# Kernel tuning notes

Measured on AMD Instinct MI355X. Metric: run time of the kernel, lower is better.

The kernel has to match this reference:

```python
import jax, jax.numpy as jnp
import numpy as np

B, H = 8192, 768


def _mk_linear(key, fan_in, fan_out):
    k1, k2 = jax.random.split(key)
    lim = 1.0 / np.sqrt(fan_in)
    W = jax.random.uniform(k1, (fan_out, fan_in), jnp.float32, -lim, lim)
    b = jax.random.uniform(k2, (fan_out,), jnp.float32, -lim, lim)
    return W, b


def setup_inputs() -> dict:
    key = jax.random.key(0)
    ks = jax.random.split(key, 6)
    modal_a = jax.random.normal(ks[0], (B, H), jnp.float32)
    modal_b = jax.random.normal(ks[1], (B, H), jnp.float32)
    W1m, b1m = _mk_linear(ks[2], H, H)
    W2m, b2m = _mk_linear(ks[3], H, H)
    W1v, b1v = _mk_linear(ks[4], H, H)
    W2v, b2v = _mk_linear(ks[5], H, H)
    return {"modal_a": modal_a, "modal_b": modal_b,
            "W1m": W1m, "b1m": b1m, "W2m": W2m, "b2m": b2m,
            "W1v": W1v, "b1v": b1v, "W2v": W2v, "b2v": b2v}


def reference(modal_a, modal_b, W1m, b1m, W2m, b2m, W1v, b1v, W2v, b2v):
    # mlp_mu: Linear -> Tanh -> Linear
    mu = jnp.tanh(modal_a @ W1m.T + b1m) @ W2m.T + b2m              # [B,H]
    # mlp_logvar: Linear -> Tanh -> Linear -> Tanh
    logvar = jnp.tanh(jnp.tanh(modal_a @ W1v.T + b1v) @ W2v.T + b2v)  # [B,H]
    inv_var = jnp.exp(-logvar)

    positive = -(mu - modal_b) ** 2 * 0.5 * inv_var                  # [B,H]

    # mean_j (mu[j] - mu[i])^2 = E[mu^2] - 2*mu[i]*E[mu] + mu[i]^2  (per feature dim)
    # Algebraic reduction of the O(B^2*H) tile in the original code.
    mu_mean = jnp.mean(mu, axis=0)                                   # [H]
    mu_sq_mean = jnp.mean(mu * mu, axis=0)                           # [H]
    pair_sq = mu_sq_mean - 2.0 * mu * mu_mean + mu * mu              # [B,H]
    negative = -pair_sq * 0.5 * inv_var                              # [B,H]

    pos_sum = jnp.sum(positive, axis=-1)                             # [B]
    neg_sum = jnp.sum(negative, axis=-1)                             # [B]
    lld = jnp.mean(pos_sum)
    bound = jnp.mean(pos_sum - neg_sum)
    return (lld, bound)
```

## Files before the change

### kernel.cpp

```cpp
#include <hip/hip_runtime.h>
#include <hip/hip_fp8.h>
#include <math.h>

typedef float v4f __attribute__((ext_vector_type(4)));

static constexpr int Bn = 8192;
static constexpr int Hn = 768;
static constexpr float invB = 1.0f / 8192.0f;

__device__ __forceinline__ unsigned char cvt_e4m3(float x) {
    __hip_fp8_e4m3 t(x);
    return t.__x;
}

__device__ __forceinline__ unsigned pack4_e4m3(float4 f) {
    return (unsigned)cvt_e4m3(f.x)
         | ((unsigned)cvt_e4m3(f.y) << 8)
         | ((unsigned)cvt_e4m3(f.z) << 16)
         | ((unsigned)cvt_e4m3(f.w) << 24);
}

__device__ __forceinline__ float fast_tanh(float x) {
    float xc = fminf(fmaxf(x, -15.0f), 15.0f);
    float e = __expf(2.0f * xc);
    float r = __builtin_amdgcn_rcpf(e + 1.0f);
    return 1.0f - 2.0f * r;
}

__global__ void prep_w(const float* __restrict__ W1m, const float* __restrict__ W2m,
                       const float* __restrict__ W1v, const float* __restrict__ W2v,
                       unsigned char* __restrict__ W1m_f8, unsigned char* __restrict__ W2m_f8,
                       unsigned char* __restrict__ W1v_f8, unsigned char* __restrict__ W2v_f8,
                       float* __restrict__ zbuf, int nzero) {
    const int tid = blockIdx.x * blockDim.x + threadIdx.x;
    if (tid < nzero) zbuf[tid] = 0.0f;
    constexpr int W4 = Hn * Hn / 4;
    const int total = 4 * W4;
    const int stride = gridDim.x * blockDim.x;
    for (int i = tid; i < total; i += stride) {
        int w = i / W4, j = i - w * W4;
        const float* s = (w == 0) ? W1m : (w == 1) ? W2m : (w == 2) ? W1v : W2v;
        unsigned char* d = (w == 0) ? W1m_f8 : (w == 1) ? W2m_f8 : (w == 2) ? W1v_f8 : W2v_f8;
        float4 v = ((const float4*)s)[j];
        ((unsigned*)d)[j] = pack4_e4m3(v);
    }
}

__launch_bounds__(1024, 4)
__global__ void club_fused(const float* __restrict__ A_g,
                           const unsigned char* __restrict__ W1m, const unsigned char* __restrict__ W1v,
                           const unsigned char* __restrict__ W2m, const unsigned char* __restrict__ W2v,
                           const float* __restrict__ b1m, const float* __restrict__ b1v,
                           const float* __restrict__ b2m, const float* __restrict__ b2v,
                           const float* __restrict__ mb,
                           float* __restrict__ cs, float* __restrict__ cs2,
                           float* __restrict__ siv, float* __restrict__ sivmu,
                           float* __restrict__ accum, float* __restrict__ outp) {
    __shared__ __align__(16) unsigned char Hm[32 * 768];
    __shared__ __align__(16) unsigned char Xs[32 * 768];
    const int t = threadIdx.x;
    const int strip0 = blockIdx.x * 32;

    for (int c = t; c < 1536; c += 1024) {
        const int row = c / 48, cc = c - row * 48;
        const float* src = A_g + (size_t)(strip0 + row) * Hn + cc * 16;
        float4 f0 = *(const float4*)(src + 0);
        float4 f1 = *(const float4*)(src + 4);
        float4 f2 = *(const float4*)(src + 8);
        float4 f3 = *(const float4*)(src + 12);
        uint4 p;
        p.x = pack4_e4m3(f0); p.y = pack4_e4m3(f1);
        p.z = pack4_e4m3(f2); p.w = pack4_e4m3(f3);
        *(uint4*)&Xs[row * 768 + ((cc ^ (row & 15)) << 4)] = p;
    }
    __syncthreads();

    const int w = t >> 6, lane = t & 63;
    const int lr = lane & 15, quad = lane >> 4;
    const int wc0 = w * 48;

    v4f am[3][2] = {}, av[3][2] = {};
    {
        const unsigned char* __restrict__ pWm = W1m + (size_t)(wc0 + lr) * Hn + quad * 16;
        const unsigned char* __restrict__ pWv = W1v + (size_t)(wc0 + lr) * Hn + quad * 16;
#pragma unroll
        for (int ms = 0; ms < 12; ++ms) {
            ulonglong2 wmf[3], wvf[3], af[2];
#pragma unroll
            for (int ct = 0; ct < 3; ++ct) {
                wmf[ct] = *(const ulonglong2*)(pWm + ct * (16 * Hn) + ms * 64);
                wvf[ct] = *(const ulonglong2*)(pWv + ct * (16 * Hn) + ms * 64);
            }
#pragma unroll
            for (int rt = 0; rt < 2; ++rt) {
                const int row_ = rt * 16 + lr;
                const int k_ = ms * 4 + quad;
                af[rt] = *(const ulonglong2*)&Xs[row_ * 768 + ((k_ ^ (row_ & 15)) << 4)];
            }
#pragma unroll
            for (int ct = 0; ct < 3; ++ct)
#pragma unroll
                for (int rt = 0; rt < 2; ++rt) {
                    am[ct][rt] = __builtin_amdgcn_mfma_f32_16x16x32_fp8_fp8((long)wmf[ct].x, (long)af[rt].x, am[ct][rt], 0, 0, 0);
                    av[ct][rt] = __builtin_amdgcn_mfma_f32_16x16x32_fp8_fp8((long)wvf[ct].x, (long)af[rt].x, av[ct][rt], 0, 0, 0);
                }
#pragma unroll
            for (int ct = 0; ct < 3; ++ct)
#pragma unroll
                for (int rt = 0; rt < 2; ++rt) {
                    am[ct][rt] = __builtin_amdgcn_mfma_f32_16x16x32_fp8_fp8((long)wmf[ct].y, (long)af[rt].y, am[ct][rt], 0, 0, 0);
                    av[ct][rt] = __builtin_amdgcn_mfma_f32_16x16x32_fp8_fp8((long)wvf[ct].y, (long)af[rt].y, av[ct][rt], 0, 0, 0);
                }
        }
    }

    __syncthreads();

#pragma unroll
    for (int ct = 0; ct < 3; ++ct) {
        const float4 bbm = *(const float4*)&b1m[wc0 + ct * 16 + quad * 4];
        const float4 bbv = *(const float4*)&b1v[wc0 + ct * 16 + quad * 4];
        const int cc = w * 3 + ct;
#pragma unroll
        for (int rt = 0; rt < 2; ++rt) {
            const int row = rt * 16 + lr;
            v4f a = am[ct][rt];
            unsigned pm = (unsigned)cvt_e4m3(fast_tanh(a[0] + bbm.x))
                        | ((unsigned)cvt_e4m3(fast_tanh(a[1] + bbm.y)) << 8)
                        | ((unsigned)cvt_e4m3(fast_tanh(a[2] + bbm.z)) << 16)
                        | ((unsigned)cvt_e4m3(fast_tanh(a[3] + bbm.w)) << 24);
            v4f b = av[ct][rt];
            unsigned pv = (unsigned)cvt_e4m3(fast_tanh(b[0] + bbv.x))
                        | ((unsigned)cvt_e4m3(fast_tanh(b[1] + bbv.y)) << 8)
                        | ((unsigned)cvt_e4m3(fast_tanh(b[2] + bbv.z)) << 16)
                        | ((unsigned)cvt_e4m3(fast_tanh(b[3] + bbv.w)) << 24);
            const int off = row * 768 + ((cc ^ (row & 15)) << 4) + quad * 4;
            *(unsigned*)&Hm[off] = pm;
            *(unsigned*)&Xs[off] = pv;
        }
    }
    __syncthreads();

    v4f cm[2][3] = {}, cv[2][3] = {};
    {
        const unsigned char* __restrict__ pWm = W2m + (size_t)(wc0 + lr) * Hn + quad * 16;
        const unsigned char* __restrict__ pWv = W2v + (size_t)(wc0 + lr) * Hn + quad * 16;
#pragma unroll
        for (int ms = 0; ms < 12; ++ms) {
            ulonglong2 wmf[3], wvf[3], amf[2], avf[2];
#pragma unroll
            for (int ct = 0; ct < 3; ++ct) {
                wmf[ct] = *(const ulonglong2*)(pWm + ct * (16 * Hn) + ms * 64);
                wvf[ct] = *(const ulonglong2*)(pWv + ct * (16 * Hn) + ms * 64);
            }
#pragma unroll
            for (int rt = 0; rt < 2; ++rt) {
                const int row_ = rt * 16 + lr;
                const int k_ = ms * 4 + quad;
                const int off_ = row_ * 768 + ((k_ ^ (row_ & 15)) << 4);
                amf[rt] = *(const ulonglong2*)&Hm[off_];
                avf[rt] = *(const ulonglong2*)&Xs[off_];
            }
#pragma unroll
            for (int rt = 0; rt < 2; ++rt)
#pragma unroll
                for (int ct = 0; ct < 3; ++ct) {
                    cm[rt][ct] = __builtin_amdgcn_mfma_f32_16x16x32_fp8_fp8((long)amf[rt].x, (long)wmf[ct].x, cm[rt][ct], 0, 0, 0);
                    cv[rt][ct] = __builtin_amdgcn_mfma_f32_16x16x32_fp8_fp8((long)avf[rt].x, (long)wvf[ct].x, cv[rt][ct], 0, 0, 0);
                }
#pragma unroll
            for (int rt = 0; rt < 2; ++rt)
#pragma unroll
                for (int ct = 0; ct < 3; ++ct) {
                    cm[rt][ct] = __builtin_amdgcn_mfma_f32_16x16x32_fp8_fp8((long)amf[rt].y, (long)wmf[ct].y, cm[rt][ct], 0, 0, 0);
                    cv[rt][ct] = __builtin_amdgcn_mfma_f32_16x16x32_fp8_fp8((long)avf[rt].y, (long)wvf[ct].y, cv[rt][ct], 0, 0, 0);
                }
        }
    }

    float pos = 0.f, q = 0.f;
#pragma unroll
    for (int ct = 0; ct < 3; ++ct) {
        const int col = wc0 + ct * 16 + lr;
        const float bmc = b2m[col], bvc = b2v[col];
        float c1 = 0.f, c2 = 0.f, c3 = 0.f, c4 = 0.f;
#pragma unroll
        for (int rt = 0; rt < 2; ++rt) {
#pragma unroll
            for (int r = 0; r < 4; ++r) {
                const int row = strip0 + rt * 16 + quad * 4 + r;
                float mu = cm[rt][ct][r] + bmc;
                float tv = fast_tanh(cv[rt][ct][r] + bvc);
                float iv = __expf(-tv);
                float mbv = mb[(size_t)row * Hn + col];
                float d = mu - mbv;
                pos += iv * d * d;
                q   += iv * mu * mu;
                c1 += mu; c2 += mu * mu; c3 += iv; c4 += iv * mu;
            }
        }
        c1 += __shfl_xor(c1, 16); c1 += __shfl_xor(c1, 32);
        c2 += __shfl_xor(c2, 16); c2 += __shfl_xor(c2, 32);
        c3 += __shfl_xor(c3, 16); c3 += __shfl_xor(c3, 32);
        c4 += __shfl_xor(c4, 16); c4 += __shfl_xor(c4, 32);
        if (quad == 0) {
            atomicAdd(&cs[col], c1);
            atomicAdd(&cs2[col], c2);
            atomicAdd(&siv[col], c3);
            atomicAdd(&sivmu[col], c4);
        }
    }
    for (int off = 32; off > 0; off >>= 1) {
        pos += __shfl_down(pos, off);
        q   += __shfl_down(q, off);
    }
    __shared__ float redP[16], redQ[16];
    if (lane == 0) { redP[w] = pos; redQ[w] = q; }
    __syncthreads();
    __shared__ int is_last;
    if (t == 0) {
        float sp = 0.f, sq = 0.f;
#pragma unroll
        for (int i = 0; i < 16; ++i) { sp += redP[i]; sq += redQ[i]; }
        atomicAdd(&accum[0], sp);
        atomicAdd(&accum[1], sq);
        __threadfence();
        unsigned old = atomicAdd((unsigned int*)&accum[3], 1u);
        is_last = (old == gridDim.x - 1) ? 1 : 0;
    }
    __syncthreads();
    if (is_last) {
        float term = 0.f;
        for (int h = t; h < Hn; h += 1024) {
            float v1 = atomicAdd(&cs[h], 0.0f);
            float v2 = atomicAdd(&cs2[h], 0.0f);
            float v3 = atomicAdd(&siv[h], 0.0f);
            float v4 = atomicAdd(&sivmu[h], 0.0f);
            term += v3 * v2 - 2.0f * v4 * v1;
        }
        for (int off = 32; off > 0; off >>= 1) term += __shfl_down(term, off);
        __shared__ float redT[16];
        if (lane == 0) redT[w] = term;
        __syncthreads();
        if (t == 0) {
            float T = 0.f;
#pragma unroll
            for (int i = 0; i < 16; ++i) T += redT[i];
            float P = atomicAdd(&accum[0], 0.0f);
            float Q = atomicAdd(&accum[1], 0.0f);
            float pos_sum = -0.5f * P;
            float neg_sum = -0.5f * (T * invB + Q);
            outp[0] = pos_sum * invB;
            outp[1] = (pos_sum - neg_sum) * invB;
        }
    }
}

extern "C" void kernel_launch(void* const* d_in, const int* in_sizes, int n_in,
                              void* d_out, int out_size, void* d_ws, size_t ws_size,
                              hipStream_t stream) {
    const float* modal_a = (const float*)d_in[0];
    const float* modal_b = (const float*)d_in[1];
    const float* W1m = (const float*)d_in[2];
    const float* b1m = (const float*)d_in[3];
    const float* W2m = (const float*)d_in[4];
    const float* b2m = (const float*)d_in[5];
    const float* W1v = (const float*)d_in[6];
    const float* b1v = (const float*)d_in[7];
    const float* W2v = (const float*)d_in[8];
    const float* b2v = (const float*)d_in[9];
    float* out = (float*)d_out;

    char* ws = (char*)d_ws;
    constexpr size_t szW8 = (size_t)Hn * Hn;
    unsigned char* W1m_f8 = (unsigned char*)(ws);
    unsigned char* W2m_f8 = (unsigned char*)(ws + szW8);
    unsigned char* W1v_f8 = (unsigned char*)(ws + 2 * szW8);
    unsigned char* W2v_f8 = (unsigned char*)(ws + 3 * szW8);
    float* cs     = (float*)(ws + 4 * szW8);
    float* cs2    = cs + Hn;
    float* siv    = cs + 2 * Hn;
    float* sivmu  = cs + 3 * Hn;
    float* accum  = cs + 4 * Hn;

    prep_w<<<576, 256, 0, stream>>>(W1m, W2m, W1v, W2v,
                                    W1m_f8, W2m_f8, W1v_f8, W2v_f8,
                                    cs, 4 * Hn + 8);

    club_fused<<<dim3(Bn / 32), 1024, 0, stream>>>(
        modal_a, W1m_f8, W1v_f8, W2m_f8, W2v_f8,
        b1m, b1v, b2m, b2v, modal_b,
        cs, cs2, siv, sivmu, accum, out);
}
```

Before: 188.0 us.

## Merge weight-quantization prep into main kernel with cooperative grid sync

```diff
diff --git a/kernel.cpp b/kernel.cpp
--- a/kernel.cpp
+++ b/kernel.cpp
@@ -1,4 +1,5 @@
 #include <hip/hip_runtime.h>
+#include <hip/hip_cooperative_groups.h>
 #include <hip/hip_fp8.h>
 #include <math.h>
 
@@ -27,39 +28,36 @@
     return 1.0f - 2.0f * r;
 }
 
-__global__ void prep_w(const float* __restrict__ W1m, const float* __restrict__ W2m,
-                       const float* __restrict__ W1v, const float* __restrict__ W2v,
-                       unsigned char* __restrict__ W1m_f8, unsigned char* __restrict__ W2m_f8,
-                       unsigned char* __restrict__ W1v_f8, unsigned char* __restrict__ W2v_f8,
-                       float* __restrict__ zbuf, int nzero) {
-    const int tid = blockIdx.x * blockDim.x + threadIdx.x;
-    if (tid < nzero) zbuf[tid] = 0.0f;
-    constexpr int W4 = Hn * Hn / 4;
-    const int total = 4 * W4;
-    const int stride = gridDim.x * blockDim.x;
-    for (int i = tid; i < total; i += stride) {
-        int w = i / W4, j = i - w * W4;
-        const float* s = (w == 0) ? W1m : (w == 1) ? W2m : (w == 2) ? W1v : W2v;
-        unsigned char* d = (w == 0) ? W1m_f8 : (w == 1) ? W2m_f8 : (w == 2) ? W1v_f8 : W2v_f8;
-        float4 v = ((const float4*)s)[j];
-        ((unsigned*)d)[j] = pack4_e4m3(v);
-    }
-}
-
 __launch_bounds__(1024, 4)
-__global__ void club_fused(const float* __restrict__ A_g,
-                           const unsigned char* __restrict__ W1m, const unsigned char* __restrict__ W1v,
-                           const unsigned char* __restrict__ W2m, const unsigned char* __restrict__ W2v,
-                           const float* __restrict__ b1m, const float* __restrict__ b1v,
-                           const float* __restrict__ b2m, const float* __restrict__ b2v,
-                           const float* __restrict__ mb,
-                           float* __restrict__ cs, float* __restrict__ cs2,
-                           float* __restrict__ siv, float* __restrict__ sivmu,
-                           float* __restrict__ accum, float* __restrict__ outp) {
+__global__ void club_all(const float* __restrict__ A_g, const float* __restrict__ mb,
+                         const float* __restrict__ W1m_f, const float* __restrict__ W2m_f,
+                         const float* __restrict__ W1v_f, const float* __restrict__ W2v_f,
+                         const float* __restrict__ b1m, const float* __restrict__ b1v,
+                         const float* __restrict__ b2m, const float* __restrict__ b2v,
+                         unsigned char* __restrict__ W1m8, unsigned char* __restrict__ W2m8,
+                         unsigned char* __restrict__ W1v8, unsigned char* __restrict__ W2v8,
+                         float* __restrict__ cs, float* __restrict__ cs2,
+                         float* __restrict__ siv, float* __restrict__ sivmu,
+                         float* __restrict__ accum, float* __restrict__ outp) {
     __shared__ __align__(16) unsigned char Hm[32 * 768];
     __shared__ __align__(16) unsigned char Xs[32 * 768];
     const int t = threadIdx.x;
     const int strip0 = blockIdx.x * 32;
+
+    {
+        const int gtid = blockIdx.x * 1024 + t;
+        if (gtid < 4 * Hn + 8) cs[gtid] = 0.0f;
+        constexpr int W4 = Hn * Hn / 4;
+        for (int i = gtid; i < 4 * W4; i += 256 * 1024) {
+            int w = i / W4, j = i - w * W4;
+            const float* s = (w == 0) ? W1m_f : (w == 1) ? W2m_f : (w == 2) ? W1v_f : W2v_f;
+            unsigned char* d = (w == 0) ? W1m8 : (w == 1) ? W2m8 : (w == 2) ? W1v8 : W2v8;
+            float4 v = ((const float4*)s)[j];
+            ((unsigned*)d)[j] = pack4_e4m3(v);
+        }
+    }
+    __threadfence();
+    cooperative_groups::this_grid().sync();
 
     for (int c = t; c < 1536; c += 1024) {
         const int row = c / 48, cc = c - row * 48;
@@ -81,8 +79,8 @@
 
     v4f am[3][2] = {}, av[3][2] = {};
     {
-        const unsigned char* __restrict__ pWm = W1m + (size_t)(wc0 + lr) * Hn + quad * 16;
-        const unsigned char* __restrict__ pWv = W1v + (size_t)(wc0 + lr) * Hn + quad * 16;
+        const unsigned char* __restrict__ pWm = W1m8 + (size_t)(wc0 + lr) * Hn + quad * 16;
+        const unsigned char* __restrict__ pWv = W1v8 + (size_t)(wc0 + lr) * Hn + quad * 16;
 #pragma unroll
         for (int ms = 0; ms < 12; ++ms) {
             ulonglong2 wmf[3], wvf[3], af[2];
@@ -143,8 +141,8 @@
 
     v4f cm[2][3] = {}, cv[2][3] = {};
     {
-        const unsigned char* __restrict__ pWm = W2m + (size_t)(wc0 + lr) * Hn + quad * 16;
-        const unsigned char* __restrict__ pWv = W2v + (size_t)(wc0 + lr) * Hn + quad * 16;
+        const unsigned char* __restrict__ pWm = W2m8 + (size_t)(wc0 + lr) * Hn + quad * 16;
+        const unsigned char* __restrict__ pWv = W2v8 + (size_t)(wc0 + lr) * Hn + quad * 16;
 #pragma unroll
         for (int ms = 0; ms < 12; ++ms) {
             ulonglong2 wmf[3], wvf[3], amf[2], avf[2];
@@ -283,12 +281,13 @@
     float* sivmu  = cs + 3 * Hn;
     float* accum  = cs + 4 * Hn;
 
-    prep_w<<<576, 256, 0, stream>>>(W1m, W2m, W1v, W2v,
-                                    W1m_f8, W2m_f8, W1v_f8, W2v_f8,
-                                    cs, 4 * Hn + 8);
-
-    club_fused<<<dim3(Bn / 32), 1024, 0, stream>>>(
-        modal_a, W1m_f8, W1v_f8, W2m_f8, W2v_f8,
-        b1m, b1v, b2m, b2v, modal_b,
-        cs, cs2, siv, sivmu, accum, out);
-}
+    void* args[] = { (void*)&modal_a, (void*)&modal_b,
+                     (void*)&W1m, (void*)&W2m, (void*)&W1v, (void*)&W2v,
+                     (void*)&b1m, (void*)&b1v, (void*)&b2m, (void*)&b2v,
+                     (void*)&W1m_f8, (void*)&W2m_f8, (void*)&W1v_f8, (void*)&W2v_f8,
+                     (void*)&cs, (void*)&cs2, (void*)&siv, (void*)&sivmu,
+                     (void*)&accum, (void*)&out };
+
+    hipLaunchCooperativeKernel((const void*)club_all, dim3(Bn / 32), dim3(1024),
+                               args, 0, stream);
+}
```

Result: slower. 302.5 us (+60.9%).

## Prefetch modal_b tile into LDS asynchronously and use nontemporal input loads

Applied to the files above, without the earlier changes.

```diff
diff --git a/kernel.cpp b/kernel.cpp
--- a/kernel.cpp
+++ b/kernel.cpp
@@ -4,6 +4,9 @@
 
 typedef float v4f __attribute__((ext_vector_type(4)));
 
+#define AS1 __attribute__((address_space(1)))
+#define AS3 __attribute__((address_space(3)))
+
 static constexpr int Bn = 8192;
 static constexpr int Hn = 768;
 static constexpr float invB = 1.0f / 8192.0f;
@@ -13,7 +16,7 @@
     return t.__x;
 }
 
-__device__ __forceinline__ unsigned pack4_e4m3(float4 f) {
+__device__ __forceinline__ unsigned pack4_e4m3(v4f f) {
     return (unsigned)cvt_e4m3(f.x)
          | ((unsigned)cvt_e4m3(f.y) << 8)
          | ((unsigned)cvt_e4m3(f.z) << 16)
@@ -41,7 +44,7 @@
         int w = i / W4, j = i - w * W4;
         const float* s = (w == 0) ? W1m : (w == 1) ? W2m : (w == 2) ? W1v : W2v;
         unsigned char* d = (w == 0) ? W1m_f8 : (w == 1) ? W2m_f8 : (w == 2) ? W1v_f8 : W2v_f8;
-        float4 v = ((const float4*)s)[j];
+        v4f v = __builtin_nontemporal_load((const v4f*)s + j);
         ((unsigned*)d)[j] = pack4_e4m3(v);
     }
 }
@@ -58,16 +61,17 @@
                            float* __restrict__ accum, float* __restrict__ outp) {
     __shared__ __align__(16) unsigned char Hm[32 * 768];
     __shared__ __align__(16) unsigned char Xs[32 * 768];
+    __shared__ __align__(16) float Mb_s[32 * 768];
     const int t = threadIdx.x;
     const int strip0 = blockIdx.x * 32;
 
     for (int c = t; c < 1536; c += 1024) {
         const int row = c / 48, cc = c - row * 48;
-        const float* src = A_g + (size_t)(strip0 + row) * Hn + cc * 16;
-        float4 f0 = *(const float4*)(src + 0);
-        float4 f1 = *(const float4*)(src + 4);
-        float4 f2 = *(const float4*)(src + 8);
-        float4 f3 = *(const float4*)(src + 12);
+        const v4f* src = (const v4f*)(A_g + (size_t)(strip0 + row) * Hn + cc * 16);
+        v4f f0 = __builtin_nontemporal_load(src + 0);
+        v4f f1 = __builtin_nontemporal_load(src + 1);
+        v4f f2 = __builtin_nontemporal_load(src + 2);
+        v4f f3 = __builtin_nontemporal_load(src + 3);
         uint4 p;
         p.x = pack4_e4m3(f0); p.y = pack4_e4m3(f1);
         p.z = pack4_e4m3(f2); p.w = pack4_e4m3(f3);
@@ -78,6 +82,18 @@
     const int w = t >> 6, lane = t & 63;
     const int lr = lane & 15, quad = lane >> 4;
     const int wc0 = w * 48;
+
+    {
+        const char* mb_base = (const char*)(mb + (size_t)strip0 * Hn);
+        char* mb_lds = (char*)Mb_s;
+#pragma unroll
+        for (int j = 0; j < 6; ++j) {
+            const int chunk = w * 6 + j;
+            __builtin_amdgcn_global_load_lds(
+                (const AS1 void*)(mb_base + chunk * 1024 + lane * 16),
+                (AS3 void*)(mb_lds + chunk * 1024 + lane * 16), 16, 0, 0);
+        }
+    }
 
     v4f am[3][2] = {}, av[3][2] = {};
     {
@@ -188,11 +204,11 @@
         for (int rt = 0; rt < 2; ++rt) {
 #pragma unroll
             for (int r = 0; r < 4; ++r) {
-                const int row = strip0 + rt * 16 + quad * 4 + r;
+                const int lrow = rt * 16 + quad * 4 + r;
                 float mu = cm[rt][ct][r] + bmc;
                 float tv = fast_tanh(cv[rt][ct][r] + bvc);
                 float iv = __expf(-tv);
-                float mbv = mb[(size_t)row * Hn + col];
+                float mbv = Mb_s[lrow * 768 + col];
                 float d = mu - mbv;
                 pos += iv * d * d;
                 q   += iv * mu * mu;
```

New measurement: 199.2 us. 1.06x slower.
